# Optimization experiments

Measured on AMD Instinct MI355X. Metric: run time of the kernel, lower is better.

## Reference

```python
import jax, jax.numpy as jnp
from jax import lax
import numpy as np

B_, T_ = 16, 8
H_, W_ = 14, 14
h_, w_ = 3, 3
N_ = h_ * w_
CB, C_, D_ = 1024, 512, 128


def setup_inputs():
    key = jax.random.key(0)
    ks = jax.random.split(key, 16)
    rn = lambda i, shp, s=0.02: jax.random.normal(ks[i], shp, dtype=jnp.float32) * s
    z = lambda *s: jnp.zeros(s, jnp.float32)
    o = lambda *s: jnp.ones(s, jnp.float32)
    return {
        'x': jax.random.normal(ks[0], (B_ * T_, CB, H_, W_), dtype=jnp.float32),
        'W_proj': rn(1, (C_, CB)), 'b_proj': z(C_),
        'W_attn': rn(2, (N_, C_)),
        'W_gf': rn(3, (D_, C_)), 'b_gf': z(D_),
        'g1': o(N_, D_), 'beta1': z(N_, D_), 'g2': o(N_, D_), 'beta2': z(N_, D_),
        'W_ih': rn(4, (4 * D_, D_)), 'W_hh': rn(5, (4 * D_, D_)), 'b_ih': z(4 * D_), 'b_hh': z(4 * D_),
        'W_pred': rn(6, (4, D_)), 'b_pred': z(4), 'alpha': jnp.full((4,), 0.5, jnp.float32),
        'W_kp1': rn(7, (C_, H_ * W_)), 'b_kp1': z(C_),
        'Wq': rn(8, (C_, C_)), 'Wk': rn(9, (C_, C_)), 'Wv': rn(10, (C_, C_)), 'Wu': rn(11, (C_, C_)), 'b_u': z(C_),
        'W_gih': rn(12, (3 * C_, C_)), 'W_ghh': rn(13, (3 * C_, C_)), 'b_gih': z(3 * C_), 'b_ghh': z(3 * C_),
        'W_back': rn(14, (CB, C_)), 'b_back': z(CB),
    }


def _ln(x, g, b, eps=1e-5):
    m = x.mean(-1, keepdims=True)
    v = x.var(-1, keepdims=True)
    return (x - m) / jnp.sqrt(v + eps) * g + b


def _forward(x, W_proj, b_proj, W_attn, W_gf, b_gf, g1, beta1, g2, beta2, W_ih, W_hh, b_ih, b_hh, W_pred, b_pred, alpha, W_kp1, b_kp1, Wq, Wk, Wv, Wu, b_u, W_gih, W_ghh, b_gih, b_ghh, W_back, b_back):
    BT = x.shape[0]
    # 1x1 conv projection backbone_dim -> node_dim (project_at_input)  [BT, C, H, W]
    feat = jnp.einsum('oc,bchw->bohw', W_proj, x) + b_proj[None, :, None, None]
    # offset generator: per-node attention pooling over space (GloRe-style)
    logits = jnp.einsum('nc,bchw->bnhw', W_attn, feat).reshape(BT, N_, H_ * W_)
    attw = jax.nn.softmax(logits, axis=-1).reshape(BT, N_, H_, W_)
    gf = jnp.einsum('bnhw,bchw->bnc', attw, feat)  # [BT, N, C]
    gf = _ln(gf @ W_gf.T + b_gf, g1, beta1)  # [BT, N, D]
    # temporal LSTM over T, batched over (B, node)
    xs = gf.reshape(B_, T_, N_, D_).transpose(1, 0, 2, 3).reshape(T_, B_ * N_, D_)
    def lstm_step(carry, xt):
        hp, cp = carry
        gates = xt @ W_ih.T + b_ih + hp @ W_hh.T + b_hh
        i, f, gg, oo = jnp.split(gates, 4, axis=-1)
        c = jax.nn.sigmoid(f) * cp + jax.nn.sigmoid(i) * jnp.tanh(gg)
        hn = jax.nn.sigmoid(oo) * jnp.tanh(c)
        return (hn, c), hn
    h0 = jnp.zeros((B_ * N_, D_), xs.dtype)
    _, ys = lax.scan(lstm_step, (h0, h0), xs)
    ys = ys.reshape(T_, B_, N_, D_).transpose(1, 0, 2, 3).reshape(BT, N_, D_)
    off = (_ln(ys, g2, beta2) @ W_pred.T + b_pred) * alpha  # [BT, N, 4]
    # grid anchors (init_regions='grid'): centers at (k+0.5)*H/h
    ph0 = (jnp.arange(h_, dtype=x.dtype) + 0.5) * (H_ / h_)
    pw0 = (jnp.arange(w_, dtype=x.dtype) + 0.5) * (W_ / w_)
    ch = jnp.repeat(ph0, w_)[None] + off[..., 0]
    cw = jnp.tile(pw0, h_)[None] + off[..., 1]
    sh = (H_ / h_) * jnp.exp(off[..., 2])
    sw = (W_ / w_) * jnp.exp(off[..., 3])
    rel_h = (jnp.arange(h_, dtype=x.dtype) + 0.5) / h_ - 0.5
    rel_w = (jnp.arange(w_, dtype=x.dtype) + 0.5) / w_ - 0.5
    pos_h = ch[..., None] + sh[..., None] * rel_h  # [BT, N, h]
    pos_w = cw[..., None] + sw[..., None] * rel_w  # [BT, N, w]
    grid_h = jnp.arange(H_, dtype=x.dtype)
    grid_w = jnp.arange(W_, dtype=x.dtype)
    kh = jax.nn.relu(1.0 - jnp.abs(pos_h[..., None] - grid_h))  # [BT, N, h, H] linear-interp kernels
    kw = jax.nn.relu(1.0 - jnp.abs(pos_w[..., None] - grid_w))  # [BT, N, w, W]
    # differentiable crop: sample h x w region per node, pool to node vector
    t1 = jnp.einsum('bniH,bcHL->bnicL', kh, feat)
    samp = jnp.einsum('bnicL,bnjL->bnicj', t1, kw).mean(axis=(2, 4))  # [BT, N, C]
    # kernel-location embedding (kernel_projection1), combine_by_sum
    kern2d = jnp.einsum('bniH,bnjL->bnHL', kh, kw).reshape(BT, N_, H_ * W_)
    nodes = samp + kern2d @ W_kp1.T + b_kp1
    # RSTG: spatial message passing on fully-connected node graph
    nd = nodes.reshape(B_, T_, N_, C_)
    q = nd @ Wq.T
    k = nd @ Wk.T
    v = nd @ Wv.T
    att = jax.nn.softmax(jnp.einsum('btic,btjc->btij', q, k) / jnp.sqrt(jnp.asarray(C_, x.dtype)), axis=-1)
    agg = jnp.einsum('btij,btjc->btic', att, v)
    nd = nd + jax.nn.relu(agg @ Wu.T + b_u)
    # RSTG: temporal GRU per node
    def gru_step(hp, xt):
        gi = xt @ W_gih.T + b_gih
        gh = hp @ W_ghh.T + b_ghh
        ir, iz, ig = jnp.split(gi, 3, axis=-1)
        hr, hz, hg = jnp.split(gh, 3, axis=-1)
        r = jax.nn.sigmoid(ir + hr)
        zz = jax.nn.sigmoid(iz + hz)
        n = jnp.tanh(ig + r * hg)
        hn = (1.0 - zz) * n + zz * hp
        return hn, hn
    g0 = jnp.zeros((B_, N_, C_), x.dtype)
    _, hs = lax.scan(gru_step, g0, nd.transpose(1, 0, 2, 3))
    out_nodes = hs.transpose(1, 0, 2, 3).reshape(BT, N_, C_)
    # remap node states back to the spatial map with the same kernels
    khs = kh.sum(2)  # [BT, N, H]
    kws = kw.sum(2)  # [BT, N, W]
    num = jnp.einsum('bnc,bnH,bnL->bcHL', out_nodes, khs, kws)
    den = jnp.einsum('bnH,bnL->bHL', khs, kws) + 1e-6
    out_map = num / den[:, None]
    # project back node_dim -> backbone_dim (project_back_i3d_linear), residual add
    return x + jnp.einsum('oc,bchw->bohw', W_back, out_map) + b_back[None, :, None, None]


def reference(x, W_proj, b_proj, W_attn, W_gf, b_gf, g1, beta1, g2, beta2, W_ih, W_hh, b_ih, b_hh, W_pred, b_pred, alpha, W_kp1, b_kp1, Wq, Wk, Wv, Wu, b_u, W_gih, W_ghh, b_gih, b_ghh, W_back, b_back):
    return _forward(x, W_proj, b_proj, W_attn, W_gf, b_gf, g1, beta1, g2, beta2, W_ih, W_hh, b_ih, b_hh, W_pred, b_pred, alpha, W_kp1, b_kp1, Wq, Wk, Wv, Wu, b_u, W_gih, W_ghh, b_gih, b_ghh, W_back, b_back)
```

## Files before the change

kernel.cpp:

```cpp
#include <hip/hip_runtime.h>

typedef unsigned short u16;
typedef __attribute__((ext_vector_type(8))) u16 b16x8;
typedef __attribute__((ext_vector_type(4))) float f32x4;

static constexpr int HWn = 196;
static constexpr int NN  = 9;
static constexpr int Cn  = 512;
static constexpr int CBn = 1024;
static constexpr int Dn  = 128;
static constexpr int BTn = 128;

__device__ __forceinline__ float sigm(float x) { return 1.f / (1.f + expf(-x)); }

__device__ __forceinline__ u16 f2bf(float f) {
  unsigned int u = __builtin_bit_cast(unsigned int, f);
  u = (u + 0x7fff + ((u >> 16) & 1)) >> 16;
  return (u16)u;
}

__device__ __forceinline__ float waveSum(float v) {
#pragma unroll
  for (int o = 32; o > 0; o >>= 1) v += __shfl_down(v, o, 64);
  return v;
}
__device__ __forceinline__ float waveMax(float v) {
#pragma unroll
  for (int o = 32; o > 0; o >>= 1) v = fmaxf(v, __shfl_down(v, o, 64));
  return v;
}
__device__ __forceinline__ float blockSum(float v, float* red) {
  const int lane = threadIdx.x & 63, wid = threadIdx.x >> 6;
  const int nw = blockDim.x >> 6;
  v = waveSum(v);
  __syncthreads();
  if (lane == 0) red[wid] = v;
  __syncthreads();
  float r = 0.f;
  for (int i = 0; i < nw; ++i) r += red[i];
  return r;
}
__device__ __forceinline__ float blockMax(float v, float* red) {
  const int lane = threadIdx.x & 63, wid = threadIdx.x >> 6;
  const int nw = blockDim.x >> 6;
  v = waveMax(v);
  __syncthreads();
  if (lane == 0) red[wid] = v;
  __syncthreads();
  float r = -3.4e38f;
  for (int i = 0; i < nw; ++i) r = fmaxf(r, red[i]);
  return r;
}

__global__ __launch_bounds__(256) void k_cast(const float* __restrict__ in,
                                              u16* __restrict__ out, int n) {
  const int i = (blockIdx.x * 256 + threadIdx.x) * 4;
  if (i < n) {
    const float4 v = *(const float4*)&in[i];
    out[i + 0] = f2bf(v.x); out[i + 1] = f2bf(v.y);
    out[i + 2] = f2bf(v.z); out[i + 3] = f2bf(v.w);
  }
}

__global__ __launch_bounds__(256) void k_castall(const float* __restrict__ wq,
                                                 const float* __restrict__ wk,
                                                 const float* __restrict__ wv,
                                                 const float* __restrict__ wu,
                                                 const float* __restrict__ wgih,
                                                 const float* __restrict__ wghh,
                                                 const float* __restrict__ wih,
                                                 u16* __restrict__ dst) {
  const int i = (blockIdx.x * 256 + threadIdx.x) * 4;
  if (i >= 2686976) return;
  const float* src;
  int o = i;
  if (i < 262144) { src = wq; }
  else if (i < 524288)  { src = wk;   o = i - 262144; }
  else if (i < 786432)  { src = wv;   o = i - 524288; }
  else if (i < 1048576) { src = wu;   o = i - 786432; }
  else if (i < 1835008) { src = wgih; o = i - 1048576; }
  else if (i < 2621440) { src = wghh; o = i - 1835008; }
  else                  { src = wih;  o = i - 2621440; }
  const float4 v = *(const float4*)&src[o];
  dst[i + 0] = f2bf(v.x); dst[i + 1] = f2bf(v.y);
  dst[i + 2] = f2bf(v.z); dst[i + 3] = f2bf(v.w);
}

__global__ __launch_bounds__(256) void k_xt(const float* __restrict__ x,
                                            u16* __restrict__ xT) {
  __shared__ u16 T[64][201];
  const int bt = blockIdx.x, c0 = blockIdx.y * 64, tid = threadIdx.x;
  const float* xb = x + ((size_t)bt * CBn + c0) * HWn;
  for (int idx = tid; idx < 64 * HWn; idx += 256)
    T[idx / HWn][idx % HWn] = f2bf(xb[idx]);
  __syncthreads();
  unsigned int* xTu = (unsigned int*)(xT + ((size_t)bt * HWn) * CBn + c0);
  for (int idx = tid; idx < HWn * 32; idx += 256) {
    const int hw = idx >> 5, j = idx & 31;
    const unsigned int lo = T[2 * j][hw], hi = T[2 * j + 1][hw];
    xTu[(size_t)hw * (CBn / 2) + j] = lo | (hi << 16);
  }
}

template <int MODE>
__global__ __launch_bounds__(256) void k_mm128(const u16* __restrict__ A,
                                               const u16* __restrict__ B,
                                               const float* __restrict__ bias,
                                               const float* __restrict__ resid,
                                               float* __restrict__ C,
                                               const int M, const int N, const int K) {
  __shared__ __align__(16) u16 As[128 * 64];
  __shared__ __align__(16) u16 Bs[128 * 64];
  const int tid = threadIdx.x;
  const int lane = tid & 63;
  const int w = tid >> 6, wr = w >> 1, wc = w & 1;
  const int m0 = blockIdx.x * 128, n0 = blockIdx.y * 128;

  int srowA[4], srowB[4], slds[4], sc16[4];
#pragma unroll
  for (int i = 0; i < 4; ++i) {
    const int chunk = i * 256 + tid;
    const int row = chunk >> 3, c16 = chunk & 7;
    srowA[i] = min(m0 + row, M - 1);
    srowB[i] = n0 + row;
    sc16[i] = c16;
    slds[i] = row * 64 + ((c16 ^ (row & 7)) << 3);
  }
  uint4 ar[4], br[4];
#pragma unroll
  for (int i = 0; i < 4; ++i) {
    ar[i] = *(const uint4*)(A + (size_t)srowA[i] * K + sc16[i] * 8);
    br[i] = *(const uint4*)(B + (size_t)srowB[i] * K + sc16[i] * 8);
  }

  int fa[4][2], fb[4][2];
#pragma unroll
  for (int q = 0; q < 4; ++q)
#pragma unroll
    for (int ks = 0; ks < 2; ++ks) {
      const int rowa = wr * 64 + q * 16 + (lane & 15);
      fa[q][ks] = rowa * 64 + (((ks * 4 + (lane >> 4)) ^ (rowa & 7)) << 3);
      const int rowb = wc * 64 + q * 16 + (lane & 15);
      fb[q][ks] = rowb * 64 + (((ks * 4 + (lane >> 4)) ^ (rowb & 7)) << 3);
    }

  f32x4 acc[4][4];
#pragma unroll
  for (int a = 0; a < 4; ++a)
#pragma unroll
    for (int b = 0; b < 4; ++b) acc[a][b] = f32x4{0.f, 0.f, 0.f, 0.f};

  for (int k0 = 0; k0 < K; k0 += 64) {
    __syncthreads();
#pragma unroll
    for (int i = 0; i < 4; ++i) {
      *(uint4*)&As[slds[i]] = ar[i];
      *(uint4*)&Bs[slds[i]] = br[i];
    }
    __syncthreads();
    const int kn = k0 + 64;
    if (kn < K) {
#pragma unroll
      for (int i = 0; i < 4; ++i) {
        ar[i] = *(const uint4*)(A + (size_t)srowA[i] * K + kn + sc16[i] * 8);
        br[i] = *(const uint4*)(B + (size_t)srowB[i] * K + kn + sc16[i] * 8);
      }
    }
    b16x8 af[4][2], bg[4][2];
#pragma unroll
    for (int q = 0; q < 4; ++q)
#pragma unroll
      for (int ks = 0; ks < 2; ++ks) {
        af[q][ks] = *(const b16x8*)&As[fa[q][ks]];
        bg[q][ks] = *(const b16x8*)&Bs[fb[q][ks]];
      }
#pragma unroll
    for (int ks = 0; ks < 2; ++ks)
#pragma unroll
      for (int mi = 0; mi < 4; ++mi)
#pragma unroll
        for (int nj = 0; nj < 4; ++nj) {
          if (MODE == 1)
            asm volatile("v_mfma_f32_16x16x32_bf16 %0, %1, %2, %0"
                         : "+v"(acc[mi][nj])
                         : "v"(bg[nj][ks]), "v"(af[mi][ks]));
          else
            asm volatile("v_mfma_f32_16x16x32_bf16 %0, %1, %2, %0"
                         : "+v"(acc[mi][nj])
                         : "v"(af[mi][ks]), "v"(bg[nj][ks]));
        }
  }

  if (MODE == 1) {
#pragma unroll
    for (int nj = 0; nj < 4; ++nj) {
#pragma unroll
      for (int r = 0; r < 4; ++r) {
        const int n = n0 + wc * 64 + nj * 16 + (lane >> 4) * 4 + r;
        const float bv = bias[n];
#pragma unroll
        for (int mi = 0; mi < 4; ++mi) {
          const int m = m0 + wr * 64 + mi * 16 + (lane & 15);
          const int b = m / HWn, hw = m - b * HWn;
          const size_t adr = ((size_t)b * CBn + n) * HWn + hw;
          C[adr] = resid[adr] + acc[mi][nj][r] + bv;
        }
      }
    }
  } else {
#pragma unroll
    for (int nj = 0; nj < 4; ++nj) {
      const int n = n0 + wc * 64 + nj * 16 + (lane & 15);
      const float bv = (MODE == 3) ? bias[n] : (bias ? bias[n] : 0.f);
#pragma unroll
      for (int mi = 0; mi < 4; ++mi) {
#pragma unroll
        for (int r = 0; r < 4; ++r) {
          const int m = m0 + wr * 64 + mi * 16 + (lane >> 4) * 4 + r;
          if (m >= M) continue;
          if (MODE == 0) {
            C[(size_t)m * N + n] = acc[mi][nj][r] + bv;
          } else {
            const float val = resid[(size_t)m * N + n] + fmaxf(acc[mi][nj][r] + bv, 0.f);
            ((u16*)C)[(size_t)m * N + n] = f2bf(val);
          }
        }
      }
    }
  }
}

__global__ __launch_bounds__(256) void k_attnpool(const float* __restrict__ feat,
                                                  const float* __restrict__ Wattn,
                                                  float* __restrict__ attw) {
  __shared__ float S[HWn][65];
  __shared__ float Wa[NN][64];
  __shared__ float L[NN][HWn];
  __shared__ float red[4];
  const int bt = blockIdx.x, tid = threadIdx.x;
  float lacc[NN];
#pragma unroll
  for (int n = 0; n < NN; ++n) lacc[n] = 0.f;
  const float* fb = feat + (size_t)bt * HWn * Cn;
  const int srow = tid >> 4, sc4 = (tid & 15) << 2;
  for (int c0 = 0; c0 < Cn; c0 += 64) {
    for (int rr = srow; rr < HWn; rr += 16) {
      const float4 f = *(const float4*)&fb[(size_t)rr * Cn + c0 + sc4];
      S[rr][sc4] = f.x; S[rr][sc4 + 1] = f.y; S[rr][sc4 + 2] = f.z; S[rr][sc4 + 3] = f.w;
    }
    for (int idx = tid; idx < NN * 64; idx += 256)
      Wa[idx >> 6][idx & 63] = Wattn[(size_t)(idx >> 6) * Cn + c0 + (idx & 63)];
    __syncthreads();
    if (tid < HWn) {
      for (int c = 0; c < 64; ++c) {
        const float s = S[tid][c];
#pragma unroll
        for (int n = 0; n < NN; ++n) lacc[n] += Wa[n][c] * s;
      }
    }
    __syncthreads();
  }
  if (tid < HWn)
#pragma unroll
    for (int n = 0; n < NN; ++n) L[n][tid] = lacc[n];
  __syncthreads();
  for (int n = 0; n < NN; ++n) {
    const float v = (tid < HWn) ? L[n][tid] : -3.4e38f;
    const float mx = blockMax(v, red);
    const float e = (tid < HWn) ? expf(v - mx) : 0.f;
    const float s = blockSum(e, red);
    if (tid < HWn) attw[((size_t)bt * NN + n) * HWn + tid] = e / s;
  }
}

__global__ __launch_bounds__(256) void k_gf(const float* __restrict__ feat,
                                            const float* __restrict__ attw,
                                            float* __restrict__ gf) {
  __shared__ float aw[NN][HWn];
  const int bt = blockIdx.x, tid = threadIdx.x;
  for (int idx = tid; idx < NN * HWn; idx += 256)
    aw[idx / HWn][idx % HWn] = attw[(size_t)bt * NN * HWn + idx];
  __syncthreads();
  float a0[NN] = {}, a1[NN] = {};
  const float* fb = feat + (size_t)bt * HWn * Cn;
  for (int hw = 0; hw < HWn; ++hw) {
    const float f0 = fb[(size_t)hw * Cn + tid];
    const float f1 = fb[(size_t)hw * Cn + tid + 256];
#pragma unroll
    for (int n = 0; n < NN; ++n) {
      const float w = aw[n][hw];
      a0[n] += w * f0; a1[n] += w * f1;
    }
  }
#pragma unroll
  for (int n = 0; n < NN; ++n) {
    gf[((size_t)bt * NN + n) * Cn + tid] = a0[n];
    gf[((size_t)bt * NN + n) * Cn + tid + 256] = a1[n];
  }
}

__global__ __launch_bounds__(128) void k_gfln(const float* __restrict__ gf,
                                              const float* __restrict__ Wgf,
                                              const float* __restrict__ bgf,
                                              const float* __restrict__ g1,
                                              const float* __restrict__ beta1,
                                              u16* __restrict__ gf2b) {
  __shared__ __align__(16) float src[Cn];
  __shared__ float red[4];
  const int row = blockIdx.x;
  const int n = row % NN;
  const int tid = threadIdx.x;
  for (int i = tid; i < Cn; i += 128) src[i] = gf[(size_t)row * Cn + i];
  __syncthreads();
  float acc = bgf[tid];
  const float* wr = Wgf + (size_t)tid * Cn;
  for (int c = 0; c < Cn; c += 4) {
    const float4 w = *(const float4*)&wr[c];
    acc += w.x * src[c] + w.y * src[c + 1] + w.z * src[c + 2] + w.w * src[c + 3];
  }
  const float mean = blockSum(acc, red) * (1.f / 128.f);
  const float d = acc - mean;
  const float var = blockSum(d * d, red) * (1.f / 128.f);
  gf2b[(size_t)row * Dn + tid] =
      f2bf(d * rsqrtf(var + 1e-5f) * g1[n * Dn + tid] + beta1[n * Dn + tid]);
}

__global__ __launch_bounds__(256) void k_lstm(const float* __restrict__ xW,
                                              const float* __restrict__ Whh,
                                              const float* __restrict__ bhh,
                                              float* __restrict__ ys) {
  __shared__ __align__(16) float h[Dn];
  __shared__ float cc[Dn];
  __shared__ float gates[4 * Dn];
  const int blk = blockIdx.x, b = blk / NN, n = blk % NN;
  const int tid = threadIdx.x;
  if (tid < Dn) { h[tid] = 0.f; cc[tid] = 0.f; }
  __syncthreads();
  for (int t = 0; t < 8; ++t) {
    const int bt = b * 8 + t;
    const size_t xrow = ((size_t)bt * NN + n) * (4 * Dn);
#pragma unroll
    for (int gq = 0; gq < 2; ++gq) {
      const int g = tid + gq * 256;
      float acc = xW[xrow + g] + bhh[g];
      const float* wr = Whh + (size_t)g * Dn;
#pragma unroll 8
      for (int d = 0; d < Dn; d += 4) {
        const float4 w = *(const float4*)&wr[d];
        acc += w.x * h[d] + w.y * h[d + 1] + w.z * h[d + 2] + w.w * h[d + 3];
      }
      gates[g] = acc;
    }
    __syncthreads();
    if (tid < Dn) {
      const float ig = sigm(gates[tid]);
      const float fg = sigm(gates[Dn + tid]);
      const float gg = tanhf(gates[2 * Dn + tid]);
      const float og = sigm(gates[3 * Dn + tid]);
      const float cn = fg * cc[tid] + ig * gg;
      const float hn = og * tanhf(cn);
      cc[tid] = cn; h[tid] = hn;
      ys[((size_t)bt * NN + n) * Dn + tid] = hn;
    }
    __syncthreads();
  }
}

__global__ __launch_bounds__(128) void k_off(const float* __restrict__ ys,
                                             const float* __restrict__ g2,
                                             const float* __restrict__ beta2,
                                             const float* __restrict__ Wpred,
                                             const float* __restrict__ bpred,
                                             const float* __restrict__ alpha,
                                             float* __restrict__ khs,
                                             float* __restrict__ kws) {
  __shared__ float red[4];
  __shared__ float cpar[4];
  const int row = blockIdx.x;
  const int n = row % NN;
  const int tid = threadIdx.x;
  const float y = ys[(size_t)row * Dn + tid];
  const float mean = blockSum(y, red) * (1.f / 128.f);
  const float d = y - mean;
  const float var = blockSum(d * d, red) * (1.f / 128.f);
  const float v = d * rsqrtf(var + 1e-5f) * g2[n * Dn + tid] + beta2[n * Dn + tid];
  const float o0 = blockSum(v * Wpred[0 * Dn + tid], red);
  const float o1 = blockSum(v * Wpred[1 * Dn + tid], red);
  const float o2 = blockSum(v * Wpred[2 * Dn + tid], red);
  const float o3 = blockSum(v * Wpred[3 * Dn + tid], red);
  if (tid == 0) {
    const float f0 = (o0 + bpred[0]) * alpha[0];
    const float f1 = (o1 + bpred[1]) * alpha[1];
    const float f2 = (o2 + bpred[2]) * alpha[2];
    const float f3 = (o3 + bpred[3]) * alpha[3];
    const float ph0 = ((n / 3) + 0.5f) * (14.f / 3.f);
    const float pw0 = ((n % 3) + 0.5f) * (14.f / 3.f);
    cpar[0] = ph0 + f0;
    cpar[1] = pw0 + f1;
    cpar[2] = (14.f / 3.f) * expf(f2);
    cpar[3] = (14.f / 3.f) * expf(f3);
  }
  __syncthreads();
  if (tid < 14) {
    float s = 0.f;
#pragma unroll
    for (int i = 0; i < 3; ++i) {
      const float rel = (i + 0.5f) / 3.f - 0.5f;
      const float p = cpar[0] + cpar[2] * rel;
      s += fmaxf(1.f - fabsf(p - (float)tid), 0.f);
    }
    khs[(size_t)row * 14 + tid] = s;
  } else if (tid < 28) {
    const int H = tid - 14;
    float s = 0.f;
#pragma unroll
    for (int i = 0; i < 3; ++i) {
      const float rel = (i + 0.5f) / 3.f - 0.5f;
      const float p = cpar[1] + cpar[3] * rel;
      s += fmaxf(1.f - fabsf(p - (float)H), 0.f);
    }
    kws[(size_t)row * 14 + H] = s;
  }
}

__global__ __launch_bounds__(256) void k_wkp1t(const float* __restrict__ Wkp1,
                                               float* __restrict__ wkT) {
  const int hw = blockIdx.x, c = threadIdx.x;
  wkT[(size_t)hw * Cn + c] = Wkp1[(size_t)c * HWn + hw];
  wkT[(size_t)hw * Cn + c + 256] = Wkp1[(size_t)(c + 256) * HWn + hw];
}

__global__ __launch_bounds__(256) void k_nodes(const float* __restrict__ feat,
                                               const float* __restrict__ wkT,
                                               const float* __restrict__ khs,
                                               const float* __restrict__ kws,
                                               const float* __restrict__ bkp1,
                                               float* __restrict__ nodes,
                                               u16* __restrict__ nodesb) {
  __shared__ float kh[NN][14], kw[NN][14];
  const int bt = blockIdx.x, tid = threadIdx.x;
  if (tid < NN * 14) {
    kh[tid / 14][tid % 14] = khs[(size_t)bt * NN * 14 + tid];
    kw[tid / 14][tid % 14] = kws[(size_t)bt * NN * 14 + tid];
  }
  __syncthreads();
  float a0[NN] = {}, a1[NN] = {};
  const float* fb = feat + (size_t)bt * HWn * Cn;
  for (int hw = 0; hw < HWn; ++hw) {
    const int Hh = hw / 14, Ll = hw % 14;
    const float f0 = fb[(size_t)hw * Cn + tid] * (1.f / 9.f) + wkT[(size_t)hw * Cn + tid];
    const float f1 = fb[(size_t)hw * Cn + tid + 256] * (1.f / 9.f) + wkT[(size_t)hw * Cn + tid + 256];
#pragma unroll
    for (int n = 0; n < NN; ++n) {
      const float w = kh[n][Hh] * kw[n][Ll];
      a0[n] += w * f0; a1[n] += w * f1;
    }
  }
#pragma unroll
  for (int n = 0; n < NN; ++n) {
    const float v0 = a0[n] + bkp1[tid];
    const float v1 = a1[n] + bkp1[tid + 256];
    nodes[((size_t)bt * NN + n) * Cn + tid] = v0;
    nodes[((size_t)bt * NN + n) * Cn + tid + 256] = v1;
    nodesb[((size_t)bt * NN + n) * Cn + tid] = f2bf(v0);
    nodesb[((size_t)bt * NN + n) * Cn + tid + 256] = f2bf(v1);
  }
}

__global__ __launch_bounds__(256) void k_att(const float* __restrict__ q,
                                             const float* __restrict__ k,
                                             const float* __restrict__ v,
                                             u16* __restrict__ aggb) {
  __shared__ __align__(16) float qs[NN][Cn];
  __shared__ __align__(16) float ks[NN][Cn];
  __shared__ __align__(16) float vs[NN][Cn];
  __shared__ float s[NN][NN];
  const int bt = blockIdx.x, tid = threadIdx.x;
  const size_t base = (size_t)bt * NN * Cn;
  for (int idx = tid; idx < NN * Cn; idx += 256) {
    qs[idx / Cn][idx % Cn] = q[base + idx];
    ks[idx / Cn][idx % Cn] = k[base + idx];
    vs[idx / Cn][idx % Cn] = v[base + idx];
  }
  __syncthreads();
  if (tid < NN * NN) {
    const int i = tid / NN, j = tid % NN;
    float acc = 0.f;
    for (int c = 0; c < Cn; c += 4) {
      const float4 qa = *(const float4*)&qs[i][c];
      const float4 kb = *(const float4*)&ks[j][c];
      acc += qa.x * kb.x + qa.y * kb.y + qa.z * kb.z + qa.w * kb.w;
    }
    s[i][j] = acc * 0.044194173824159216f;
  }
  __syncthreads();
  if (tid < NN) {
    float mx = -3.4e38f;
#pragma unroll
    for (int j = 0; j < NN; ++j) mx = fmaxf(mx, s[tid][j]);
    float sum = 0.f;
#pragma unroll
    for (int j = 0; j < NN; ++j) { const float e = expf(s[tid][j] - mx); s[tid][j] = e; sum += e; }
    const float inv = 1.f / sum;
#pragma unroll
    for (int j = 0; j < NN; ++j) s[tid][j] *= inv;
  }
  __syncthreads();
  for (int c = tid; c < Cn; c += 256) {
#pragma unroll
    for (int i = 0; i < NN; ++i) {
      float acc = 0.f;
#pragma unroll
      for (int j = 0; j < NN; ++j) acc += s[i][j] * vs[j][c];
      aggb[((size_t)bt * NN + i) * Cn + c] = f2bf(acc);
    }
  }
}

template <int T0>
__global__ __launch_bounds__(256) void k_gruupd(const float* __restrict__ gi,
                                                const float* __restrict__ gh,
                                                const float* __restrict__ bghh,
                                                float* __restrict__ hgru,
                                                u16* __restrict__ hb,
                                                float* __restrict__ out_nodes,
                                                int t) {
  const int idx = blockIdx.x * 256 + threadIdx.x;
  const int row = idx >> 9, d = idx & 511;
  const int b = row / NN, n = row % NN;
  const size_t girow = ((size_t)(b * 8 + t) * NN + n) * (3 * Cn);
  const float ir = gi[girow + d], iz = gi[girow + Cn + d], ig = gi[girow + 2 * Cn + d];
  float hr, hz, hg, hp;
  if (T0) {
    hr = bghh[d]; hz = bghh[Cn + d]; hg = bghh[2 * Cn + d]; hp = 0.f;
  } else {
    const size_t gr = (size_t)row * (3 * Cn);
    hr = gh[gr + d]; hz = gh[gr + Cn + d]; hg = gh[gr + 2 * Cn + d];
    hp = hgru[(size_t)row * Cn + d];
  }
  const float rg = sigm(ir + hr);
  const float zg = sigm(iz + hz);
  const float ng = tanhf(ig + rg * hg);
  const float h = (1.f - zg) * ng + zg * hp;
  hgru[(size_t)row * Cn + d] = h;
  hb[(size_t)row * Cn + d] = f2bf(h);
  out_nodes[((size_t)(b * 8 + t) * NN + n) * Cn + d] = h;
}

__global__ __launch_bounds__(256) void k_remap(const float* __restrict__ out_nodes,
                                               const float* __restrict__ khs,
                                               const float* __restrict__ kws,
                                               u16* __restrict__ om) {
  __shared__ __align__(16) float on[NN][Cn];
  __shared__ float kh[NN][14], kw[NN][14];
  const int bt = blockIdx.x, tid = threadIdx.x;
  for (int idx = tid; idx < NN * Cn; idx += 256)
    on[idx / Cn][idx % Cn] = out_nodes[(size_t)bt * NN * Cn + idx];
  if (tid < NN * 14) {
    kh[tid / 14][tid % 14] = khs[(size_t)bt * NN * 14 + tid];
    kw[tid / 14][tid % 14] = kws[(size_t)bt * NN * 14 + tid];
  }
  __syncthreads();
  for (int hw = 0; hw < HWn; ++hw) {
    const int Hh = hw / 14, Ll = hw % 14;
    float w[NN];
    float den = 1e-6f;
#pragma unroll
    for (int n = 0; n < NN; ++n) { w[n] = kh[n][Hh] * kw[n][Ll]; den += w[n]; }
    const float inv = 1.f / den;
    float s0 = 0.f, s1 = 0.f;
#pragma unroll
    for (int n = 0; n < NN; ++n) {
      s0 += on[n][tid] * w[n];
      s1 += on[n][tid + 256] * w[n];
    }
    om[((size_t)bt * HWn + hw) * Cn + tid] = f2bf(s0 * inv);
    om[((size_t)bt * HWn + hw) * Cn + tid + 256] = f2bf(s1 * inv);
  }
}

extern "C" void kernel_launch(void* const* d_in, const int* in_sizes, int n_in,
                              void* d_out, int out_size, void* d_ws, size_t ws_size,
                              hipStream_t stream) {
  const float* x      = (const float*)d_in[0];
  const float* W_proj = (const float*)d_in[1];
  const float* b_proj = (const float*)d_in[2];
  const float* W_attn = (const float*)d_in[3];
  const float* W_gf   = (const float*)d_in[4];
  const float* b_gf   = (const float*)d_in[5];
  const float* g1     = (const float*)d_in[6];
  const float* beta1  = (const float*)d_in[7];
  const float* g2     = (const float*)d_in[8];
  const float* beta2  = (const float*)d_in[9];
  const float* W_ih   = (const float*)d_in[10];
  const float* W_hh   = (const float*)d_in[11];
  const float* b_ih   = (const float*)d_in[12];
  const float* b_hh   = (const float*)d_in[13];
  const float* W_pred = (const float*)d_in[14];
  const float* b_pred = (const float*)d_in[15];
  const float* alpha  = (const float*)d_in[16];
  const float* W_kp1  = (const float*)d_in[17];
  const float* b_kp1  = (const float*)d_in[18];
  const float* Wq     = (const float*)d_in[19];
  const float* Wk     = (const float*)d_in[20];
  const float* Wv     = (const float*)d_in[21];
  const float* Wu     = (const float*)d_in[22];
  const float* b_u    = (const float*)d_in[23];
  const float* W_gih  = (const float*)d_in[24];
  const float* W_ghh  = (const float*)d_in[25];
  const float* b_gih  = (const float*)d_in[26];
  const float* b_ghh  = (const float*)d_in[27];
  const float* W_back = (const float*)d_in[28];
  const float* b_back = (const float*)d_in[29];
  float* out = (float*)d_out;

  float* ws = (float*)d_ws;
  float* feat = ws;
  u16* om16 = (u16*)feat;
  float* pool = ws + 12845056;
  u16* xT = (u16*)pool;
  size_t off = 0;
  float* attw      = pool + off; off += (size_t)BTn * NN * HWn;
  float* gf        = pool + off; off += (size_t)BTn * NN * Cn;
  u16*   gf2b      = (u16*)(pool + off); off += (size_t)BTn * NN * Dn;
  float* xW        = pool + off; off += (size_t)BTn * NN * 512;
  float* ys        = pool + off; off += (size_t)BTn * NN * Dn;
  float* khs       = pool + off; off += (size_t)BTn * NN * 14;
  float* kws       = pool + off; off += (size_t)BTn * NN * 14;
  float* nodes     = pool + off; off += (size_t)BTn * NN * Cn;
  float* qb        = pool + off; off += (size_t)BTn * NN * Cn;
  float* kb        = pool + off; off += (size_t)BTn * NN * Cn;
  float* vb        = pool + off; off += (size_t)BTn * NN * Cn;
  float* gi        = pool + off; off += (size_t)BTn * NN * 3 * Cn;
  float* hgru      = pool + off; off += (size_t)144 * Cn;
  float* gh        = pool + off; off += (size_t)144 * 3 * Cn;
  float* wkT       = pool + off; off += (size_t)HWn * Cn;
  float* out_nodes = pool + off; off += (size_t)BTn * NN * Cn;
  u16* midw    = (u16*)(pool + off); off += 1343488;
  u16* nodesb  = (u16*)(pool + off); off += 294912;
  u16* nd2b    = (u16*)(pool + off); off += 294912;
  u16* aggb16  = (u16*)(pool + off); off += 294912;
  u16* hb      = (u16*)(pool + off); off += 36864;
  u16* Wqb   = midw;
  u16* Wkb   = midw + 262144;
  u16* Wvb   = midw + 524288;
  u16* Wub   = midw + 786432;
  u16* Wgihb = midw + 1048576;
  u16* Wghhb = midw + 1835008;
  u16* Wihb  = midw + 2621440;
  u16* Wpb = (u16*)(ws + 25690112);
  u16* Wbb = (u16*)(ws + 25690112 + 262144);

  k_cast<<<512, 256, 0, stream>>>(W_proj, Wpb, 524288);
  k_cast<<<512, 256, 0, stream>>>(W_back, Wbb, 524288);
  k_xt<<<dim3(128, 16), 256, 0, stream>>>(x, xT);
  k_mm128<0><<<dim3(196, 4), 256, 0, stream>>>(xT, Wpb, b_proj, nullptr, feat, 25088, 512, 1024);
  k_castall<<<2624, 256, 0, stream>>>(Wq, Wk, Wv, Wu, W_gih, W_ghh, W_ih, midw);
  k_attnpool<<<BTn, 256, 0, stream>>>(feat, W_attn, attw);
  k_gf<<<BTn, 256, 0, stream>>>(feat, attw, gf);
  k_gfln<<<BTn * NN, 128, 0, stream>>>(gf, W_gf, b_gf, g1, beta1, gf2b);
  k_mm128<0><<<dim3(9, 4), 256, 0, stream>>>(gf2b, Wihb, b_ih, nullptr, xW, 1152, 512, 128);
  k_lstm<<<144, 256, 0, stream>>>(xW, W_hh, b_hh, ys);
  k_off<<<BTn * NN, 128, 0, stream>>>(ys, g2, beta2, W_pred, b_pred, alpha, khs, kws);
  k_wkp1t<<<HWn, 256, 0, stream>>>(W_kp1, wkT);
  k_nodes<<<BTn, 256, 0, stream>>>(feat, wkT, khs, kws, b_kp1, nodes, nodesb);
  k_mm128<0><<<dim3(9, 4), 256, 0, stream>>>(nodesb, Wqb, nullptr, nullptr, qb, 1152, 512, 512);
  k_mm128<0><<<dim3(9, 4), 256, 0, stream>>>(nodesb, Wkb, nullptr, nullptr, kb, 1152, 512, 512);
  k_mm128<0><<<dim3(9, 4), 256, 0, stream>>>(nodesb, Wvb, nullptr, nullptr, vb, 1152, 512, 512);
  k_att<<<BTn, 256, 0, stream>>>(qb, kb, vb, aggb16);
  k_mm128<3><<<dim3(9, 4), 256, 0, stream>>>(aggb16, Wub, b_u, nodes, (float*)nd2b, 1152, 512, 512);
  k_mm128<0><<<dim3(9, 12), 256, 0, stream>>>(nd2b, Wgihb, b_gih, nullptr, gi, 1152, 1536, 512);
  for (int t = 0; t < 8; ++t) {
    if (t > 0)
      k_mm128<0><<<dim3(2, 12), 256, 0, stream>>>(hb, Wghhb, b_ghh, nullptr, gh, 144, 1536, 512);
    if (t == 0)
      k_gruupd<1><<<288, 256, 0, stream>>>(gi, gh, b_ghh, hgru, hb, out_nodes, t);
    else
      k_gruupd<0><<<288, 256, 0, stream>>>(gi, gh, b_ghh, hgru, hb, out_nodes, t);
  }
  k_remap<<<BTn, 256, 0, stream>>>(out_nodes, khs, kws, om16);
  k_mm128<1><<<dim3(196, 8), 256, 0, stream>>>(om16, Wbb, b_back, x, out, 25088, 1024, 512);
}
```

Before: 1.431 ms.

## Fuse GRU recurrence into one kernel, merge QKV GEMM, stage GEMM epilogues via LDS

Replaces the per-timestep GRU loop (hidden GEMM plus update kernels) with a single persistent kernel per row. Each kernel holds h in shared memory and computes W_hh·h from a pre-packed bf16 weight layout. The Q/K/V projections become one GEMM with N=1536, and attention reads from the interleaved output. GEMM epilogues for modes 0 and 1 now go through LDS for coalesced float4 stores, which matters most for the large NCHW residual output. In exchange the GRU matvec runs on scalar FMAs with only 144 blocks, and the layout and buffer sizes change in several places.

Measured after the change: 1.230 ms. 1.16x faster.

```diff
diff --git a/kernel.cpp b/kernel.cpp
--- a/kernel.cpp
+++ b/kernel.cpp
@@ -17,6 +17,12 @@
   unsigned int u = __builtin_bit_cast(unsigned int, f);
   u = (u + 0x7fff + ((u >> 16) & 1)) >> 16;
   return (u16)u;
+}
+__device__ __forceinline__ float bfhi(unsigned int u) {
+  return __builtin_bit_cast(float, u & 0xffff0000u);
+}
+__device__ __forceinline__ float bflo(unsigned int u) {
+  return __builtin_bit_cast(float, u << 16);
 }
 
 __device__ __forceinline__ float waveSum(float v) {
@@ -67,11 +73,10 @@
                                                  const float* __restrict__ wv,
                                                  const float* __restrict__ wu,
                                                  const float* __restrict__ wgih,
-                                                 const float* __restrict__ wghh,
                                                  const float* __restrict__ wih,
                                                  u16* __restrict__ dst) {
   const int i = (blockIdx.x * 256 + threadIdx.x) * 4;
-  if (i >= 2686976) return;
+  if (i >= 1900544) return;
   const float* src;
   int o = i;
   if (i < 262144) { src = wq; }
@@ -79,11 +84,20 @@
   else if (i < 786432)  { src = wv;   o = i - 524288; }
   else if (i < 1048576) { src = wu;   o = i - 786432; }
   else if (i < 1835008) { src = wgih; o = i - 1048576; }
-  else if (i < 2621440) { src = wghh; o = i - 1835008; }
-  else                  { src = wih;  o = i - 2621440; }
+  else                  { src = wih;  o = i - 1835008; }
   const float4 v = *(const float4*)&src[o];
   dst[i + 0] = f2bf(v.x); dst[i + 1] = f2bf(v.y);
   dst[i + 2] = f2bf(v.z); dst[i + 3] = f2bf(v.w);
+}
+
+__global__ __launch_bounds__(256) void k_wpack(const float* __restrict__ W,
+                                               unsigned int* __restrict__ W3) {
+  const int idx = blockIdx.x * 256 + threadIdx.x;
+  if (idx >= 393216) return;
+  const int cp = idx / 1536, j = idx % 1536;
+  const float lo = W[(size_t)j * 512 + 2 * cp];
+  const float hi = W[(size_t)j * 512 + 2 * cp + 1];
+  W3[(size_t)cp * 1536 + j] = (unsigned int)f2bf(lo) | ((unsigned int)f2bf(hi) << 16);
 }
 
 __global__ __launch_bounds__(256) void k_xt(const float* __restrict__ x,
@@ -106,11 +120,12 @@
 __global__ __launch_bounds__(256) void k_mm128(const u16* __restrict__ A,
                                                const u16* __restrict__ B,
                                                const float* __restrict__ bias,
-                                               const float* __restrict__ resid,
+                                               const float* __restrict__ xres,
                                                float* __restrict__ C,
                                                const int M, const int N, const int K) {
-  __shared__ __align__(16) u16 As[128 * 64];
-  __shared__ __align__(16) u16 Bs[128 * 64];
+  __shared__ __align__(16) u16 SM[16896];
+  u16* As = SM;
+  u16* Bs = SM + 128 * 64;
   const int tid = threadIdx.x;
   const int lane = tid & 63;
   const int w = tid >> 6, wr = w >> 1, wc = w & 1;
@@ -191,39 +206,86 @@
         }
   }
 
-  if (MODE == 1) {
-#pragma unroll
-    for (int nj = 0; nj < 4; ++nj) {
-#pragma unroll
-      for (int r = 0; r < 4; ++r) {
-        const int n = n0 + wc * 64 + nj * 16 + (lane >> 4) * 4 + r;
+  __syncthreads();
+  float* Ct = (float*)SM;
+
+  if (MODE == 0) {
+#pragma unroll
+    for (int p = 0; p < 2; ++p) {
+      if (wr == p) {
+#pragma unroll
+        for (int mi = 0; mi < 4; ++mi)
+#pragma unroll
+          for (int nj = 0; nj < 4; ++nj)
+#pragma unroll
+            for (int r = 0; r < 4; ++r)
+              Ct[wc * (64 * 66) + (mi * 16 + (lane >> 4) * 4 + r) * 66 +
+                 nj * 16 + (lane & 15)] = acc[mi][nj][r];
+      }
+      __syncthreads();
+#pragma unroll
+      for (int it = 0; it < 8; ++it) {
+        const int f = it * 256 + tid;
+        const int mr = f >> 5, nc = (f & 31) * 4;
+        const int m = m0 + p * 64 + mr;
+        if (m < M) {
+          const int half = nc >> 6, nl = nc & 63;
+          const float* src = &Ct[half * (64 * 66) + mr * 66 + nl];
+          float4 v = make_float4(src[0], src[1], src[2], src[3]);
+          if (bias) {
+            const float4 bv = *(const float4*)&bias[n0 + nc];
+            v.x += bv.x; v.y += bv.y; v.z += bv.z; v.w += bv.w;
+          }
+          *(float4*)&C[(size_t)m * N + n0 + nc] = v;
+        }
+      }
+      __syncthreads();
+    }
+  } else if (MODE == 1) {
+#pragma unroll
+    for (int p = 0; p < 2; ++p) {
+      if (wc == p) {
+#pragma unroll
+        for (int mi = 0; mi < 4; ++mi)
+#pragma unroll
+          for (int nj = 0; nj < 4; ++nj)
+#pragma unroll
+            for (int r = 0; r < 4; ++r)
+              Ct[wr * (64 * 66) + (nj * 16 + (lane >> 4) * 4 + r) * 66 +
+                 mi * 16 + (lane & 15)] = acc[mi][nj][r];
+      }
+      __syncthreads();
+#pragma unroll
+      for (int it = 0; it < 8; ++it) {
+        const int f = it * 256 + tid;
+        const int nr = f >> 5, mc = (f & 31) * 4;
+        const int n = n0 + p * 64 + nr;
+        const int m = m0 + mc;
+        const int half = mc >> 6, ml = mc & 63;
+        const float* src = &Ct[half * (64 * 66) + nr * 66 + ml];
         const float bv = bias[n];
-#pragma unroll
-        for (int mi = 0; mi < 4; ++mi) {
-          const int m = m0 + wr * 64 + mi * 16 + (lane & 15);
-          const int b = m / HWn, hw = m - b * HWn;
-          const size_t adr = ((size_t)b * CBn + n) * HWn + hw;
-          C[adr] = resid[adr] + acc[mi][nj][r] + bv;
-        }
-      }
+        const int b = m / HWn, hw = m - b * HWn;
+        const size_t adr = ((size_t)b * CBn + n) * HWn + hw;
+        const float4 xr = *(const float4*)&xres[adr];
+        float4 v = make_float4(src[0] + xr.x + bv, src[1] + xr.y + bv,
+                               src[2] + xr.z + bv, src[3] + xr.w + bv);
+        *(float4*)&C[adr] = v;
+      }
+      __syncthreads();
     }
   } else {
 #pragma unroll
     for (int nj = 0; nj < 4; ++nj) {
       const int n = n0 + wc * 64 + nj * 16 + (lane & 15);
-      const float bv = (MODE == 3) ? bias[n] : (bias ? bias[n] : 0.f);
+      const float bv = bias[n];
 #pragma unroll
       for (int mi = 0; mi < 4; ++mi) {
 #pragma unroll
         for (int r = 0; r < 4; ++r) {
           const int m = m0 + wr * 64 + mi * 16 + (lane >> 4) * 4 + r;
           if (m >= M) continue;
-          if (MODE == 0) {
-            C[(size_t)m * N + n] = acc[mi][nj][r] + bv;
-          } else {
-            const float val = resid[(size_t)m * N + n] + fmaxf(acc[mi][nj][r] + bv, 0.f);
-            ((u16*)C)[(size_t)m * N + n] = f2bf(val);
-          }
+          const float val = xres[(size_t)m * N + n] + fmaxf(acc[mi][nj][r] + bv, 0.f);
+          ((u16*)C)[(size_t)m * N + n] = f2bf(val);
         }
       }
     }
@@ -467,20 +529,19 @@
   }
 }
 
-__global__ __launch_bounds__(256) void k_att(const float* __restrict__ q,
-                                             const float* __restrict__ k,
-                                             const float* __restrict__ v,
+__global__ __launch_bounds__(256) void k_att(const float* __restrict__ qkv,
                                              u16* __restrict__ aggb) {
   __shared__ __align__(16) float qs[NN][Cn];
   __shared__ __align__(16) float ks[NN][Cn];
   __shared__ __align__(16) float vs[NN][Cn];
   __shared__ float s[NN][NN];
   const int bt = blockIdx.x, tid = threadIdx.x;
-  const size_t base = (size_t)bt * NN * Cn;
+  const size_t base = (size_t)bt * NN * 1536;
   for (int idx = tid; idx < NN * Cn; idx += 256) {
-    qs[idx / Cn][idx % Cn] = q[base + idx];
-    ks[idx / Cn][idx % Cn] = k[base + idx];
-    vs[idx / Cn][idx % Cn] = v[base + idx];
+    const int i = idx / Cn, c = idx % Cn;
+    qs[i][c] = qkv[base + (size_t)i * 1536 + c];
+    ks[i][c] = qkv[base + (size_t)i * 1536 + 512 + c];
+    vs[i][c] = qkv[base + (size_t)i * 1536 + 1024 + c];
   }
   __syncthreads();
   if (tid < NN * NN) {
@@ -517,34 +578,39 @@
   }
 }
 
-template <int T0>
-__global__ __launch_bounds__(256) void k_gruupd(const float* __restrict__ gi,
-                                                const float* __restrict__ gh,
-                                                const float* __restrict__ bghh,
-                                                float* __restrict__ hgru,
-                                                u16* __restrict__ hb,
-                                                float* __restrict__ out_nodes,
-                                                int t) {
-  const int idx = blockIdx.x * 256 + threadIdx.x;
-  const int row = idx >> 9, d = idx & 511;
-  const int b = row / NN, n = row % NN;
-  const size_t girow = ((size_t)(b * 8 + t) * NN + n) * (3 * Cn);
-  const float ir = gi[girow + d], iz = gi[girow + Cn + d], ig = gi[girow + 2 * Cn + d];
-  float hr, hz, hg, hp;
-  if (T0) {
-    hr = bghh[d]; hz = bghh[Cn + d]; hg = bghh[2 * Cn + d]; hp = 0.f;
-  } else {
-    const size_t gr = (size_t)row * (3 * Cn);
-    hr = gh[gr + d]; hz = gh[gr + Cn + d]; hg = gh[gr + 2 * Cn + d];
-    hp = hgru[(size_t)row * Cn + d];
-  }
-  const float rg = sigm(ir + hr);
-  const float zg = sigm(iz + hz);
-  const float ng = tanhf(ig + rg * hg);
-  const float h = (1.f - zg) * ng + zg * hp;
-  hgru[(size_t)row * Cn + d] = h;
-  hb[(size_t)row * Cn + d] = f2bf(h);
-  out_nodes[((size_t)(b * 8 + t) * NN + n) * Cn + d] = h;
+__global__ __launch_bounds__(512) void k_gru(const float* __restrict__ gi,
+                                             const unsigned int* __restrict__ W3,
+                                             const float* __restrict__ bghh,
+                                             float* __restrict__ out_nodes) {
+  __shared__ float h[Cn];
+  const int row = blockIdx.x, b = row / NN, n = row % NN;
+  const int d = threadIdx.x;
+  float hcur = 0.f;
+  h[d] = 0.f;
+  const float br = bghh[d], bz = bghh[Cn + d], bg = bghh[2 * Cn + d];
+  __syncthreads();
+  for (int t = 0; t < 8; ++t) {
+    float ar = br, az = bz, ag = bg;
+#pragma unroll 4
+    for (int cp = 0; cp < 256; ++cp) {
+      const float h0 = h[2 * cp], h1 = h[2 * cp + 1];
+      const unsigned int wru = W3[(size_t)cp * 1536 + d];
+      const unsigned int wzu = W3[(size_t)cp * 1536 + 512 + d];
+      const unsigned int wgu = W3[(size_t)cp * 1536 + 1024 + d];
+      ar += bflo(wru) * h0 + bfhi(wru) * h1;
+      az += bflo(wzu) * h0 + bfhi(wzu) * h1;
+      ag += bflo(wgu) * h0 + bfhi(wgu) * h1;
+    }
+    const size_t girow = ((size_t)(b * 8 + t) * NN + n) * 1536;
+    const float r = sigm(gi[girow + d] + ar);
+    const float z = sigm(gi[girow + Cn + d] + az);
+    const float g = tanhf(gi[girow + 2 * Cn + d] + r * ag);
+    const float hn = (1.f - z) * g + z * hcur;
+    __syncthreads();
+    h[d] = hn; hcur = hn;
+    out_nodes[((size_t)(b * 8 + t) * NN + n) * Cn + d] = hn;
+    __syncthreads();
+  }
 }
 
 __global__ __launch_bounds__(256) void k_remap(const float* __restrict__ out_nodes,
@@ -622,32 +688,25 @@
   size_t off = 0;
   float* attw      = pool + off; off += (size_t)BTn * NN * HWn;
   float* gf        = pool + off; off += (size_t)BTn * NN * Cn;
-  u16*   gf2b      = (u16*)(pool + off); off += (size_t)BTn * NN * Dn;
+  u16*   gf2b      = (u16*)(pool + off); off += (size_t)BTn * NN * Dn / 2 + 64;
   float* xW        = pool + off; off += (size_t)BTn * NN * 512;
   float* ys        = pool + off; off += (size_t)BTn * NN * Dn;
   float* khs       = pool + off; off += (size_t)BTn * NN * 14;
   float* kws       = pool + off; off += (size_t)BTn * NN * 14;
   float* nodes     = pool + off; off += (size_t)BTn * NN * Cn;
-  float* qb        = pool + off; off += (size_t)BTn * NN * Cn;
-  float* kb        = pool + off; off += (size_t)BTn * NN * Cn;
-  float* vb        = pool + off; off += (size_t)BTn * NN * Cn;
+  float* qkv       = pool + off; off += (size_t)BTn * NN * 1536;
   float* gi        = pool + off; off += (size_t)BTn * NN * 3 * Cn;
-  float* hgru      = pool + off; off += (size_t)144 * Cn;
-  float* gh        = pool + off; off += (size_t)144 * 3 * Cn;
   float* wkT       = pool + off; off += (size_t)HWn * Cn;
   float* out_nodes = pool + off; off += (size_t)BTn * NN * Cn;
-  u16* midw    = (u16*)(pool + off); off += 1343488;
-  u16* nodesb  = (u16*)(pool + off); off += 294912;
-  u16* nd2b    = (u16*)(pool + off); off += 294912;
-  u16* aggb16  = (u16*)(pool + off); off += 294912;
-  u16* hb      = (u16*)(pool + off); off += 36864;
-  u16* Wqb   = midw;
-  u16* Wkb   = midw + 262144;
-  u16* Wvb   = midw + 524288;
+  u16* midw    = (u16*)(pool + off); off += 950272;
+  u16* nodesb  = (u16*)(pool + off); off += 147456;
+  u16* nd2b    = (u16*)(pool + off); off += 147456;
+  u16* aggb16  = (u16*)(pool + off); off += 147456;
+  unsigned int* W3 = (unsigned int*)(pool + off); off += 393216;
+  u16* Wqkvb = midw;
   u16* Wub   = midw + 786432;
   u16* Wgihb = midw + 1048576;
-  u16* Wghhb = midw + 1835008;
-  u16* Wihb  = midw + 2621440;
+  u16* Wihb  = midw + 1835008;
   u16* Wpb = (u16*)(ws + 25690112);
   u16* Wbb = (u16*)(ws + 25690112 + 262144);
 
@@ -655,7 +714,8 @@
   k_cast<<<512, 256, 0, stream>>>(W_back, Wbb, 524288);
   k_xt<<<dim3(128, 16), 256, 0, stream>>>(x, xT);
   k_mm128<0><<<dim3(196, 4), 256, 0, stream>>>(xT, Wpb, b_proj, nullptr, feat, 25088, 512, 1024);
-  k_castall<<<2624, 256, 0, stream>>>(Wq, Wk, Wv, Wu, W_gih, W_ghh, W_ih, midw);
+  k_castall<<<1856, 256, 0, stream>>>(Wq, Wk, Wv, Wu, W_gih, W_ih, midw);
+  k_wpack<<<1536, 256, 0, stream>>>(W_ghh, W3);
   k_attnpool<<<BTn, 256, 0, stream>>>(feat, W_attn, attw);
   k_gf<<<BTn, 256, 0, stream>>>(feat, attw, gf);
   k_gfln<<<BTn * NN, 128, 0, stream>>>(gf, W_gf, b_gf, g1, beta1, gf2b);
@@ -664,20 +724,11 @@
   k_off<<<BTn * NN, 128, 0, stream>>>(ys, g2, beta2, W_pred, b_pred, alpha, khs, kws);
   k_wkp1t<<<HWn, 256, 0, stream>>>(W_kp1, wkT);
   k_nodes<<<BTn, 256, 0, stream>>>(feat, wkT, khs, kws, b_kp1, nodes, nodesb);
-  k_mm128<0><<<dim3(9, 4), 256, 0, stream>>>(nodesb, Wqb, nullptr, nullptr, qb, 1152, 512, 512);
-  k_mm128<0><<<dim3(9, 4), 256, 0, stream>>>(nodesb, Wkb, nullptr, nullptr, kb, 1152, 512, 512);
-  k_mm128<0><<<dim3(9, 4), 256, 0, stream>>>(nodesb, Wvb, nullptr, nullptr, vb, 1152, 512, 512);
-  k_att<<<BTn, 256, 0, stream>>>(qb, kb, vb, aggb16);
+  k_mm128<0><<<dim3(9, 12), 256, 0, stream>>>(nodesb, Wqkvb, nullptr, nullptr, qkv, 1152, 1536, 512);
+  k_att<<<BTn, 256, 0, stream>>>(qkv, aggb16);
   k_mm128<3><<<dim3(9, 4), 256, 0, stream>>>(aggb16, Wub, b_u, nodes, (float*)nd2b, 1152, 512, 512);
   k_mm128<0><<<dim3(9, 12), 256, 0, stream>>>(nd2b, Wgihb, b_gih, nullptr, gi, 1152, 1536, 512);
-  for (int t = 0; t < 8; ++t) {
-    if (t > 0)
-      k_mm128<0><<<dim3(2, 12), 256, 0, stream>>>(hb, Wghhb, b_ghh, nullptr, gh, 144, 1536, 512);
-    if (t == 0)
-      k_gruupd<1><<<288, 256, 0, stream>>>(gi, gh, b_ghh, hgru, hb, out_nodes, t);
-    else
-      k_gruupd<0><<<288, 256, 0, stream>>>(gi, gh, b_ghh, hgru, hb, out_nodes, t);
-  }
+  k_gru<<<144, 512, 0, stream>>>(gi, W3, b_ghh, out_nodes);
   k_remap<<<BTn, 256, 0, stream>>>(out_nodes, khs, kws, om16);
   k_mm128<1><<<dim3(196, 8), 256, 0, stream>>>(om16, Wbb, b_back, x, out, 25088, 1024, 512);
 }
```
